# Kernel tuning notes

Measured on AMD Instinct MI355X. Metric: run time of the kernel, lower is better.

The kernel has to match this reference:

```python
import jax, jax.numpy as jnp
import numpy as np

DN = ('NDHWC', 'DHWIO', 'NDHWC')
EPS = 1e-5  # torch BatchNorm default

def _conv(x, w, s):
    # Minkowski conv, kernel 3 centered: output coord j gathers input coords s*j + {-1,0,1}
    return jax.lax.conv_general_dilated(x, w, (s, s, s), ((1, 1),) * 3, dimension_numbers=DN)

def _convt(x, w):
    # stride-2 transpose conv, kernel 3 centered: output p gets input c where 2c in {p-1,p,p+1}
    return jax.lax.conv_general_dilated(x, w, (1, 1, 1), ((1, 2),) * 3,
                                        lhs_dilation=(2, 2, 2), dimension_numbers=DN)

def _down(m):
    # stride-2 coordinate map: a coarse voxel is active iff any of its 2x2x2 fine voxels is
    B, G = m.shape[0], m.shape[1]
    return m.reshape(B, G // 2, 2, G // 2, 2, G // 2, 2).any(axis=(2, 4, 6))

def _mbn(h, m, g, b):
    # MinkowskiBatchNorm: BatchNorm1d over the active (sparse) feature rows only
    mf = m[..., None].astype(h.dtype)
    h = h * mf
    cnt = jnp.maximum(jnp.sum(mf), 1.0)
    mean = jnp.sum(h, axis=(0, 1, 2, 3)) / cnt
    var = jnp.sum(((h - mean) * mf) ** 2, axis=(0, 1, 2, 3)) / cnt
    return ((h - mean) * jax.lax.rsqrt(var + EPS) * g + b) * mf


def setup_inputs() -> dict:
    key = jax.random.key(0)
    ks = jax.random.split(key, 8)
    B, G, Cin, Cout = 2, 64, 4, 16
    def w(k, shape, fan):
        return jax.random.normal(k, shape, jnp.float32) * np.float32(1.0 / np.sqrt(fan))
    return {
        'x': jax.random.normal(ks[0], (B, G, G, G, Cin), jnp.float32),
        'mask': jax.random.bernoulli(ks[1], 0.1, (B, G, G, G)),
        'w1': w(ks[2], (3, 3, 3, Cin, 8), 27 * Cin), 'g1': jnp.ones(8), 'b1': jnp.zeros(8),
        'w2': w(ks[3], (3, 3, 3, 8, 16), 27 * 8), 'g2': jnp.ones(16), 'b2': jnp.zeros(16),
        'w3': w(ks[4], (3, 3, 3, 16, 32), 27 * 16), 'g3': jnp.ones(32), 'b3': jnp.zeros(32),
        'w3t': w(ks[5], (3, 3, 3, 32, 16), 27 * 32), 'g3t': jnp.ones(16), 'b3t': jnp.zeros(16),
        'w2t': w(ks[6], (3, 3, 3, 32, 16), 27 * 32), 'g2t': jnp.ones(16), 'b2t': jnp.zeros(16),
        'w1x1': w(ks[7], (24, Cout), 24),
    }


def reference(x, mask, w1, g1, b1, w2, g2, b2, w3, g3, b3,
              w3t, g3t, b3t, w2t, g2t, b2t, w1x1):
    m1 = mask
    m2 = _down(m1)
    m4 = _down(m2)
    mf1 = m1[..., None].astype(x.dtype)

    xs = x * mf1                                      # sparse tensor: zero at inactive coords
    s1 = _mbn(_conv(xs, w1, 1), m1, g1, b1)           # block1, stride 1
    o = jax.nn.relu(s1)
    s2 = _mbn(_conv(o, w2, 2), m2, g2, b2)            # block2, stride 2
    o = jax.nn.relu(s2)
    s4 = _mbn(_conv(o, w3, 2), m4, g3, b3)            # block3, stride 4
    o = jax.nn.relu(s4)

    o = jax.nn.relu(_mbn(_convt(o, w3t), m2, g3t, b3t))   # block3_tr -> stride-2 coords
    o = jnp.concatenate([o, s2], axis=-1)                 # ME.cat(out, out_s2) -> 32 ch
    o = jax.nn.relu(_mbn(_convt(o, w2t), m1, g2t, b2t))   # block2_tr -> stride-1 coords
    o = jnp.concatenate([o, s1], axis=-1)                 # ME.cat(out, out_s1) -> 24 ch
    return jnp.einsum('bdhwc,co->bdhwo', o, w1x1) * mf1   # conv1_tr: 1x1x1 conv
```

## Files before the change

### kernel.cpp

```cpp
#include <hip/hip_runtime.h>

#define NVOX1 524288
#define NVOX2 65536
#define NVOX4 8192

#define ST_SUM1 16
#define ST_SQ1  24
#define ST_SUM2 32
#define ST_SQ2  48
#define ST_SUM3 64
#define ST_SQ3  96
#define ST_SUM3T 128
#define ST_SQ3T  144
#define ST_SUM2T 160
#define ST_SQ2T  176
#define FLAG_OFF 200
#define IC_N1 204
#define IC_N2 205
#define IC_N4 206
#define ST_ZERO 256

#define OFF_M1C 512
#define OFF_M2  (OFF_M1C + NVOX1)
#define OFF_M4  (OFF_M2 + NVOX2)
#define OFF_H1  (OFF_M4 + NVOX4)
#define OFF_S2  (OFF_H1 + NVOX1 * 8)
#define OFF_H3  (OFF_S2 + NVOX2 * 16)
#define OFF_T3  (OFF_H3 + NVOX4 * 32)
#define OFF_L1  (OFF_T3 + NVOX2 * 16)
#define OFF_L2  (OFF_L1 + NVOX1)
#define OFF_L4  (OFF_L2 + NVOX2)
#define OFF_BC1 (OFF_L4 + NVOX4)
#define OFF_BC2 (OFF_BC1 + 2048)
#define OFF_BC4 (OFF_BC2 + 256)
#define OFF_NB1  (OFF_BC4 + 32)
#define OFF_NB2  (OFF_NB1 + NVOX1)
#define OFF_NB4  (OFF_NB2 + NVOX2)
#define OFF_NBT3 (OFF_NB4 + NVOX4)
#define OFF_NBT2 (OFF_NBT3 + NVOX2)

#define EPSBN 1e-5f

__device__ __forceinline__ void ttaps(int p, int gin, int* c, int* k, int* ok) {
  c[0] = p >> 1; k[0] = (p & 1) ? 0 : 1; ok[0] = 1;
  int cb = (p + 1) >> 1;
  int o = (p & 1) && (cb < gin);
  c[1] = o ? cb : 0; k[1] = 2; ok[1] = o;
}

__device__ __forceinline__ void stat_flush8(float* sum, float* sq, float* s_sum, float* s_sq, int t) {
#pragma unroll
  for (int off = 1; off < 64; off <<= 1)
#pragma unroll
    for (int c = 0; c < 8; c++) {
      sum[c] += __shfl_xor(sum[c], off, 64);
      sq[c]  += __shfl_xor(sq[c], off, 64);
    }
  if ((t & 63) == 0) {
#pragma unroll
    for (int c = 0; c < 8; c++) { atomicAdd(&s_sum[c], sum[c]); atomicAdd(&s_sq[c], sq[c]); }
  }
}

__global__ __launch_bounds__(256) void k_detect(const unsigned int* __restrict__ m,
                                                int* __restrict__ flags) {
  int tid = blockIdx.x * 256 + threadIdx.x;
  int hasf = 0, hasb = 0;
  for (int i = tid; i < NVOX1; i += 256 * 256) {
    unsigned int v = m[i];
    if (v == 0x3F800000u) hasf = 1;
    else if (v > 1u) hasb = 1;
  }
  hasf = __syncthreads_or(hasf);
  hasb = __syncthreads_or(hasb);
  if (threadIdx.x == 0) {
    if (hasf) atomicOr(&flags[0], 1);
    if (hasb) atomicOr(&flags[1], 1);
  }
}

__global__ __launch_bounds__(256) void k_canon(const void* __restrict__ mraw,
                                               int* __restrict__ m1c,
                                               const int* __restrict__ flags,
                                               int* __restrict__ blkcnt1) {
  int idx = blockIdx.x * 256 + threadIdx.x;
  int isf = flags[0], isb = flags[1];
  int v;
  if (isf)      v = (((const float*)mraw)[idx] != 0.f);
  else if (isb) v = (((const unsigned char*)mraw)[idx] != 0);
  else          v = (((const int*)mraw)[idx] != 0);
  m1c[idx] = v;
  int c = __syncthreads_count(v);
  if (threadIdx.x == 0) blkcnt1[blockIdx.x] = c;
}

__global__ __launch_bounds__(256) void k_down1(const int* __restrict__ m1,
                                               int* __restrict__ m2,
                                               int* __restrict__ blkcnt2) {
  int idx = blockIdx.x * 256 + threadIdx.x;
  int x = idx & 31, y = (idx >> 5) & 31, z = (idx >> 10) & 31, b = idx >> 15;
  int any = 0;
#pragma unroll
  for (int dz = 0; dz < 2; dz++)
#pragma unroll
    for (int dy = 0; dy < 2; dy++)
#pragma unroll
      for (int dx = 0; dx < 2; dx++)
        any |= m1[((b * 64 + 2 * z + dz) * 64 + 2 * y + dy) * 64 + 2 * x + dx];
  any = any ? 1 : 0;
  m2[idx] = any;
  int c = __syncthreads_count(any);
  if (threadIdx.x == 0) blkcnt2[blockIdx.x] = c;
}

__global__ __launch_bounds__(256) void k_down2(const int* __restrict__ m2,
                                               int* __restrict__ m4,
                                               int* __restrict__ blkcnt4) {
  int idx = blockIdx.x * 256 + threadIdx.x;
  int x = idx & 15, y = (idx >> 4) & 15, z = (idx >> 8) & 15, b = idx >> 12;
  int any = 0;
#pragma unroll
  for (int dz = 0; dz < 2; dz++)
#pragma unroll
    for (int dy = 0; dy < 2; dy++)
#pragma unroll
      for (int dx = 0; dx < 2; dx++)
        any |= m2[((b * 32 + 2 * z + dz) * 32 + 2 * y + dy) * 32 + 2 * x + dx];
  any = any ? 1 : 0;
  m4[idx] = any;
  int c = __syncthreads_count(any);
  if (threadIdx.x == 0) blkcnt4[blockIdx.x] = c;
}

__global__ __launch_bounds__(1024) void k_scan(int* __restrict__ bc1,
                                               int* __restrict__ bc2,
                                               int* __restrict__ bc4,
                                               int* __restrict__ cnts) {
  __shared__ int sA[2048], sB[2048];
  int* a; int n; int outIdx;
  if (blockIdx.x == 0)      { a = bc1; n = 2048; outIdx = IC_N1; }
  else if (blockIdx.x == 1) { a = bc2; n = 256;  outIdx = IC_N2; }
  else                      { a = bc4; n = 32;   outIdx = IC_N4; }
  int t = threadIdx.x;
  int i0 = t, i1 = t + 1024;
  int v0 = (i0 < n) ? a[i0] : 0;
  int v1 = (i1 < n) ? a[i1] : 0;
  sA[i0] = v0; sA[i1] = v1;
  __syncthreads();
  int* src = sA; int* dst = sB;
  for (int st = 1; st < 2048; st <<= 1) {
    int x0 = src[i0]; if (i0 >= st) x0 += src[i0 - st];
    int x1 = src[i1]; if (i1 >= st) x1 += src[i1 - st];
    dst[i0] = x0; dst[i1] = x1;
    __syncthreads();
    int* tmp = src; src = dst; dst = tmp;
  }
  if (i0 < n) a[i0] = src[i0] - v0;
  if (i1 < n) a[i1] = src[i1] - v1;
  if (t == 0) cnts[outIdx] = src[2047];
}

__global__ __launch_bounds__(256) void k_scatter(const int* __restrict__ m1,
                                                 const int* __restrict__ m2,
                                                 const int* __restrict__ m4,
                                                 const int* __restrict__ bc1,
                                                 const int* __restrict__ bc2,
                                                 const int* __restrict__ bc4,
                                                 int* __restrict__ list1,
                                                 int* __restrict__ list2,
                                                 int* __restrict__ list4) {
  __shared__ int s_w[4];
  int bid = blockIdx.x, t = threadIdx.x;
  const int* mask; const int* base; int* list; int lb;
  if (bid < 2048)      { mask = m1; base = bc1; list = list1; lb = bid; }
  else if (bid < 2304) { mask = m2; base = bc2; list = list2; lb = bid - 2048; }
  else                 { mask = m4; base = bc4; list = list4; lb = bid - 2304; }
  int idx = lb * 256 + t;
  int act = mask[idx];
  unsigned long long b = __ballot(act != 0);
  int lane = t & 63, wid = t >> 6;
  if (lane == 0) s_w[wid] = __popcll(b);
  __syncthreads();
  int wbase = 0;
  for (int i = 0; i < wid; i++) wbase += s_w[i];
  if (act) {
    int pre = __popcll(b & ((1ull << lane) - 1ull));
    list[base[lb] + wbase + pre] = idx;
  }
}

__global__ __launch_bounds__(256) void k_nbr(const int* __restrict__ m1,
                                             const int* __restrict__ m2,
                                             const int* __restrict__ m4,
                                             const int* __restrict__ list1,
                                             const int* __restrict__ list2,
                                             const int* __restrict__ list4,
                                             const int* __restrict__ cnts,
                                             int* __restrict__ nb1,
                                             int* __restrict__ nb2,
                                             int* __restrict__ nb4,
                                             int* __restrict__ nbt3,
                                             int* __restrict__ nbt2) {
  int mode = blockIdx.y;
  int tid = blockIdx.x * 256 + threadIdx.x;
  int stride = gridDim.x * 256;
  if (mode == 0) {
    int n = cnts[IC_N1];
    for (int i = tid; i < n; i += stride) {
      int v = list1[i];
      int vx = v & 63, vy = (v >> 6) & 63, vz = (v >> 12) & 63, vb = v >> 18;
      unsigned wbits = 0; int tap = 0;
#pragma unroll
      for (int kd = 0; kd < 3; kd++) { int d = vz + kd - 1; int okd = ((unsigned)d < 64u); int dc = okd ? d : 0;
#pragma unroll
        for (int kh = 0; kh < 3; kh++) { int h = vy + kh - 1; int okh = ((unsigned)h < 64u); int hc = okh ? h : 0;
#pragma unroll
          for (int kw = 0; kw < 3; kw++) { int ww = vx + kw - 1; int okw = ((unsigned)ww < 64u); int wc = okw ? ww : 0;
            int ni = ((vb * 64 + dc) * 64 + hc) * 64 + wc;
            int bit = (okd & okh & okw) & (m1[ni] != 0);
            wbits |= ((unsigned)bit) << tap; tap++;
          } } }
      nb1[i] = (int)wbits;
    }
  } else if (mode == 1) {
    int n = cnts[IC_N2];
    for (int i = tid; i < n; i += stride) {
      int v = list2[i];
      int vx = v & 31, vy = (v >> 5) & 31, vz = (v >> 10) & 31, vb = v >> 15;
      unsigned wbits = 0; int tap = 0;
#pragma unroll
      for (int kd = 0; kd < 3; kd++) { int d = 2 * vz + kd - 1; int okd = (d >= 0); int dc = okd ? d : 0;
#pragma unroll
        for (int kh = 0; kh < 3; kh++) { int h = 2 * vy + kh - 1; int okh = (h >= 0); int hc = okh ? h : 0;
#pragma unroll
          for (int kw = 0; kw < 3; kw++) { int ww = 2 * vx + kw - 1; int okw = (ww >= 0); int wc = okw ? ww : 0;
            int ni = ((vb * 64 + dc) * 64 + hc) * 64 + wc;
            int bit = (okd & okh & okw) & (m1[ni] != 0);
            wbits |= ((unsigned)bit) << tap; tap++;
          } } }
      nb2[i] = (int)wbits;
    }
  } else if (mode == 2) {
    int n = cnts[IC_N4];
    for (int i = tid; i < n; i += stride) {
      int v = list4[i];
      int vx = v & 15, vy = (v >> 4) & 15, vz = (v >> 8) & 15, vb = v >> 12;
      unsigned wbits = 0; int tap = 0;
#pragma unroll
      for (int kd = 0; kd < 3; kd++) { int d = 2 * vz + kd - 1; int okd = (d >= 0); int dc = okd ? d : 0;
#pragma unroll
        for (int kh = 0; kh < 3; kh++) { int h = 2 * vy + kh - 1; int okh = (h >= 0); int hc = okh ? h : 0;
#pragma unroll
          for (int kw = 0; kw < 3; kw++) { int ww = 2 * vx + kw - 1; int okw = (ww >= 0); int wc = okw ? ww : 0;
            int ni = ((vb * 32 + dc) * 32 + hc) * 32 + wc;
            int bit = (okd & okh & okw) & (m2[ni] != 0);
            wbits |= ((unsigned)bit) << tap; tap++;
          } } }
      nb4[i] = (int)wbits;
    }
  } else if (mode == 3) {
    int n = cnts[IC_N2];
    for (int i = tid; i < n; i += stride) {
      int v = list2[i];
      int px = v & 31, py = (v >> 5) & 31, pz = (v >> 10) & 31, vb = v >> 15;
      int czv[2], kzv[2], okz[2], cyv[2], kyv[2], oky[2], cxv[2], kxv[2], okx[2];
      ttaps(pz, 16, czv, kzv, okz);
      ttaps(py, 16, cyv, kyv, oky);
      ttaps(px, 16, cxv, kxv, okx);
      unsigned wbits = 0; int comb = 0;
#pragma unroll
      for (int dz = 0; dz < 2; dz++)
#pragma unroll
        for (int dy = 0; dy < 2; dy++)
#pragma unroll
          for (int dx = 0; dx < 2; dx++) {
            int ni = ((vb * 16 + czv[dz]) * 16 + cyv[dy]) * 16 + cxv[dx];
            int bit = (okz[dz] & oky[dy] & okx[dx]) & (m4[ni] != 0);
            wbits |= ((unsigned)bit) << comb; comb++;
          }
      nbt3[i] = (int)wbits;
    }
  } else {
    int n = cnts[IC_N1];
    for (int i = tid; i < n; i += stride) {
      int v = list1[i];
      int px = v & 63, py = (v >> 6) & 63, pz = (v >> 12) & 63, vb = v >> 18;
      int czv[2], kzv[2], okz[2], cyv[2], kyv[2], oky[2], cxv[2], kxv[2], okx[2];
      ttaps(pz, 32, czv, kzv, okz);
      ttaps(py, 32, cyv, kyv, oky);
      ttaps(px, 32, cxv, kxv, okx);
      unsigned wbits = 0; int comb = 0;
#pragma unroll
      for (int dz = 0; dz < 2; dz++)
#pragma unroll
        for (int dy = 0; dy < 2; dy++)
#pragma unroll
          for (int dx = 0; dx < 2; dx++) {
            int ni = ((vb * 32 + czv[dz]) * 32 + cyv[dy]) * 32 + cxv[dx];
            int bit = (okz[dz] & oky[dy] & okx[dx]) & (m2[ni] != 0);
            wbits |= ((unsigned)bit) << comb; comb++;
          }
      nbt2[i] = (int)wbits;
    }
  }
}

__global__ __launch_bounds__(256) void k_conv1(const float* __restrict__ x,
                                               const int* __restrict__ nb1,
                                               const int* __restrict__ list1,
                                               const int* __restrict__ cnts,
                                               const float* __restrict__ w,
                                               float* __restrict__ h1,
                                               float* __restrict__ stats) {
  __shared__ float s_w[27 * 32];
  __shared__ float s_sum[8], s_sq[8];
  int t = threadIdx.x;
  { const float4* w4 = (const float4*)w; float4* sw4 = (float4*)s_w;
    for (int i = t; i < 216; i += 256) sw4[i] = w4[i]; }
  if (t < 8) { s_sum[t] = 0.f; s_sq[t] = 0.f; }
  __syncthreads();
  int n = cnts[IC_N1];
  float sum[8], sq[8];
#pragma unroll
  for (int c = 0; c < 8; c++) { sum[c] = 0.f; sq[c] = 0.f; }
  for (int i = blockIdx.x * 256 + t; i < n; i += gridDim.x * 256) {
    int v = list1[i];
    unsigned nbr = (unsigned)nb1[i];
    int vx = v & 63, vy = (v >> 6) & 63, vz = (v >> 12) & 63, vb = v >> 18;
    float acc[8];
#pragma unroll
    for (int c = 0; c < 8; c++) acc[c] = 0.f;
    int tap = 0;
#pragma unroll
    for (int kd = 0; kd < 3; kd++)
#pragma unroll
      for (int kh = 0; kh < 3; kh++)
#pragma unroll
        for (int kw = 0; kw < 3; kw++) {
          if (nbr & (1u << tap)) {
            int ni = ((vb * 64 + vz + kd - 1) * 64 + vy + kh - 1) * 64 + vx + kw - 1;
            float4 ip = *(const float4*)(x + (size_t)ni * 4);
            const float* wp = s_w + tap * 32;
#pragma unroll
            for (int co = 0; co < 8; co++) {
              float a = fmaf(ip.x, wp[co], acc[co]);
              a = fmaf(ip.y, wp[8 + co], a);
              a = fmaf(ip.z, wp[16 + co], a);
              acc[co] = fmaf(ip.w, wp[24 + co], a);
            }
          }
          tap++;
        }
    float4* hp = (float4*)(h1 + (size_t)v * 8);
    hp[0] = make_float4(acc[0], acc[1], acc[2], acc[3]);
    hp[1] = make_float4(acc[4], acc[5], acc[6], acc[7]);
#pragma unroll
    for (int c = 0; c < 8; c++) { sum[c] += acc[c]; sq[c] += acc[c] * acc[c]; }
  }
  stat_flush8(sum, sq, s_sum, s_sq, t);
  __syncthreads();
  if (t < 8) {
    if (s_sum[t] != 0.f) atomicAdd(&stats[ST_SUM1 + t], s_sum[t]);
    if (s_sq[t]  != 0.f) atomicAdd(&stats[ST_SQ1 + t], s_sq[t]);
  }
}

__global__ __launch_bounds__(256) void k_conv2(const float* __restrict__ h1,
                                               const int* __restrict__ nb2,
                                               const int* __restrict__ list2,
                                               const int* __restrict__ cnts,
                                               const float* __restrict__ w,
                                               const float* __restrict__ g1,
                                               const float* __restrict__ b1,
                                               float* __restrict__ s2,
                                               float* __restrict__ stats) {
  __shared__ float s_w[27 * 8 * 8];
  __shared__ float s_sc[8], s_bi[8];
  __shared__ float s_sum[8], s_sq[8];
  int t = threadIdx.x, g = blockIdx.y;
  for (int i = t; i < 432; i += 256) {
    int r = i >> 1, half = i & 1;
    *(float4*)(s_w + r * 8 + half * 4) = *(const float4*)(w + r * 16 + g * 8 + half * 4);
  }
  if (t < 8) {
    float cnt = fmaxf((float)cnts[IC_N1], 1.f);
    float mean = stats[ST_SUM1 + t] / cnt;
    float var = fmaxf(stats[ST_SQ1 + t] / cnt - mean * mean, 0.f);
    float sc = g1[t] * rsqrtf(var + EPSBN);
    s_sc[t] = sc; s_bi[t] = b1[t] - mean * sc;
    s_sum[t] = 0.f; s_sq[t] = 0.f;
  }
  __syncthreads();
  int n = cnts[IC_N2];
  float sum[8], sq[8];
#pragma unroll
  for (int c = 0; c < 8; c++) { sum[c] = 0.f; sq[c] = 0.f; }
  for (int i = blockIdx.x * 256 + t; i < n; i += gridDim.x * 256) {
    int v = list2[i];
    unsigned nbr = (unsigned)nb2[i];
    int vx = v & 31, vy = (v >> 5) & 31, vz = (v >> 10) & 31, vb = v >> 15;
    float acc[8];
#pragma unroll
    for (int c = 0; c < 8; c++) acc[c] = 0.f;
    int tap = 0;
#pragma unroll
    for (int kd = 0; kd < 3; kd++)
#pragma unroll
      for (int kh = 0; kh < 3; kh++)
#pragma unroll
        for (int kw = 0; kw < 3; kw++) {
          if (nbr & (1u << tap)) {
            int ni = ((vb * 64 + 2 * vz + kd - 1) * 64 + 2 * vy + kh - 1) * 64 + 2 * vx + kw - 1;
            float4 i0 = *(const float4*)(h1 + (size_t)ni * 8);
            float4 i1 = *(const float4*)(h1 + (size_t)ni * 8 + 4);
            float r[8] = {i0.x, i0.y, i0.z, i0.w, i1.x, i1.y, i1.z, i1.w};
            const float* wp = s_w + tap * 64;
#pragma unroll
            for (int ci = 0; ci < 8; ci++) {
              float vv = fmaxf(fmaf(r[ci], s_sc[ci], s_bi[ci]), 0.f);
#pragma unroll
              for (int co = 0; co < 8; co++) acc[co] = fmaf(vv, wp[ci * 8 + co], acc[co]);
            }
          }
          tap++;
        }
    float4* sp = (float4*)(s2 + (size_t)v * 16 + g * 8);
    sp[0] = make_float4(acc[0], acc[1], acc[2], acc[3]);
    sp[1] = make_float4(acc[4], acc[5], acc[6], acc[7]);
#pragma unroll
    for (int c = 0; c < 8; c++) { sum[c] += acc[c]; sq[c] += acc[c] * acc[c]; }
  }
  stat_flush8(sum, sq, s_sum, s_sq, t);
  __syncthreads();
  if (t < 8) {
    if (s_sum[t] != 0.f) atomicAdd(&stats[ST_SUM2 + g * 8 + t], s_sum[t]);
    if (s_sq[t]  != 0.f) atomicAdd(&stats[ST_SQ2 + g * 8 + t], s_sq[t]);
  }
}

__global__ __launch_bounds__(256) void k_conv3(const float* __restrict__ s2raw,
                                               const int* __restrict__ nb4,
                                               const int* __restrict__ list4,
                                               const int* __restrict__ cnts,
                                               const float* __restrict__ w,
                                               const float* __restrict__ g2,
                                               const float* __restrict__ b2,
                                               float* __restrict__ h3,
                                               float* __restrict__ stats) {
  __shared__ float s_w[27 * 16 * 8];
  __shared__ float s_sc[16], s_bi[16];
  __shared__ float s_sum[8], s_sq[8];
  int t = threadIdx.x, g = blockIdx.y;
  for (int i = t; i < 864; i += 256) {
    int r = i >> 1, half = i & 1;
    *(float4*)(s_w + r * 8 + half * 4) = *(const float4*)(w + r * 32 + g * 8 + half * 4);
  }
  if (t < 16) {
    float cnt = fmaxf((float)cnts[IC_N2], 1.f);
    float mean = stats[ST_SUM2 + t] / cnt;
    float var = fmaxf(stats[ST_SQ2 + t] / cnt - mean * mean, 0.f);
    float sc = g2[t] * rsqrtf(var + EPSBN);
    s_sc[t] = sc; s_bi[t] = b2[t] - mean * sc;
  }
  if (t < 8) { s_sum[t] = 0.f; s_sq[t] = 0.f; }
  __syncthreads();
  int n = cnts[IC_N4];
  float sum[8], sq[8];
#pragma unroll
  for (int c = 0; c < 8; c++) { sum[c] = 0.f; sq[c] = 0.f; }
  for (int i = blockIdx.x * 256 + t; i < n; i += gridDim.x * 256) {
    int v = list4[i];
    unsigned nbr = (unsigned)nb4[i];
    int vx = v & 15, vy = (v >> 4) & 15, vz = (v >> 8) & 15, vb = v >> 12;
    float acc[8];
#pragma unroll
    for (int c = 0; c < 8; c++) acc[c] = 0.f;
    int tap = 0;
#pragma unroll
    for (int kd = 0; kd < 3; kd++)
#pragma unroll
      for (int kh = 0; kh < 3; kh++)
#pragma unroll
        for (int kw = 0; kw < 3; kw++) {
          if (nbr & (1u << tap)) {
            int ni = ((vb * 32 + 2 * vz + kd - 1) * 32 + 2 * vy + kh - 1) * 32 + 2 * vx + kw - 1;
            const float4* ip = (const float4*)(s2raw + (size_t)ni * 16);
            const float* wp = s_w + tap * 128;
#pragma unroll
            for (int cq = 0; cq < 4; cq++) {
              float4 q = ip[cq];
              float rr[4] = {q.x, q.y, q.z, q.w};
#pragma unroll
              for (int j = 0; j < 4; j++) {
                int ci = cq * 4 + j;
                float vv = fmaxf(fmaf(rr[j], s_sc[ci], s_bi[ci]), 0.f);
#pragma unroll
                for (int co = 0; co < 8; co++) acc[co] = fmaf(vv, wp[ci * 8 + co], acc[co]);
              }
            }
          }
          tap++;
        }
    float4* hp = (float4*)(h3 + (size_t)v * 32 + g * 8);
    hp[0] = make_float4(acc[0], acc[1], acc[2], acc[3]);
    hp[1] = make_float4(acc[4], acc[5], acc[6], acc[7]);
#pragma unroll
    for (int c = 0; c < 8; c++) { sum[c] += acc[c]; sq[c] += acc[c] * acc[c]; }
  }
  stat_flush8(sum, sq, s_sum, s_sq, t);
  __syncthreads();
  if (t < 8) {
    if (s_sum[t] != 0.f) atomicAdd(&stats[ST_SUM3 + g * 8 + t], s_sum[t]);
    if (s_sq[t]  != 0.f) atomicAdd(&stats[ST_SQ3 + g * 8 + t], s_sq[t]);
  }
}

__global__ __launch_bounds__(256) void k_convt3(const float* __restrict__ h3raw,
                                                const int* __restrict__ nbt3,
                                                const int* __restrict__ list2,
                                                const int* __restrict__ cnts,
                                                const float* __restrict__ w,
                                                const float* __restrict__ g3,
                                                const float* __restrict__ b3,
                                                float* __restrict__ t3,
                                                float* __restrict__ stats) {
  __shared__ float s_w[27 * 32 * 8];
  __shared__ float s_sc[32], s_bi[32];
  __shared__ float s_sum[8], s_sq[8];
  int t = threadIdx.x, g = blockIdx.y;
  for (int i = t; i < 1728; i += 256) {
    int r = i >> 1, half = i & 1;
    *(float4*)(s_w + r * 8 + half * 4) = *(const float4*)(w + r * 16 + g * 8 + half * 4);
  }
  if (t < 32) {
    float cnt = fmaxf((float)cnts[IC_N4], 1.f);
    float mean = stats[ST_SUM3 + t] / cnt;
    float var = fmaxf(stats[ST_SQ3 + t] / cnt - mean * mean, 0.f);
    float sc = g3[t] * rsqrtf(var + EPSBN);
    s_sc[t] = sc; s_bi[t] = b3[t] - mean * sc;
  }
  if (t < 8) { s_sum[t] = 0.f; s_sq[t] = 0.f; }
  __syncthreads();
  int n = cnts[IC_N2];
  float sum[8], sq[8];
#pragma unroll
  for (int c = 0; c < 8; c++) { sum[c] = 0.f; sq[c] = 0.f; }
  for (int i = blockIdx.x * 256 + t; i < n; i += gridDim.x * 256) {
    int v = list2[i];
    unsigned nbr = (unsigned)nbt3[i];
    int px = v & 31, py = (v >> 5) & 31, pz = (v >> 10) & 31, vb = v >> 15;
    int czv[2], kzv[2], okz[2], cyv[2], kyv[2], oky[2], cxv[2], kxv[2], okx[2];
    ttaps(pz, 16, czv, kzv, okz);
    ttaps(py, 16, cyv, kyv, oky);
    ttaps(px, 16, cxv, kxv, okx);
    float acc[8];
#pragma unroll
    for (int c = 0; c < 8; c++) acc[c] = 0.f;
    int comb = 0;
#pragma unroll
    for (int dz = 0; dz < 2; dz++)
#pragma unroll
      for (int dy = 0; dy < 2; dy++)
#pragma unroll
        for (int dx = 0; dx < 2; dx++) {
          if (nbr & (1u << comb)) {
            int ni = ((vb * 16 + czv[dz]) * 16 + cyv[dy]) * 16 + cxv[dx];
            const float4* ip = (const float4*)(h3raw + (size_t)ni * 32);
            const float* wp = s_w + ((kzv[dz] * 3 + kyv[dy]) * 3 + kxv[dx]) * 256;
#pragma unroll
            for (int cq = 0; cq < 8; cq++) {
              float4 q = ip[cq];
              float rr[4] = {q.x, q.y, q.z, q.w};
#pragma unroll
              for (int j = 0; j < 4; j++) {
                int ci = cq * 4 + j;
                float vv = fmaxf(fmaf(rr[j], s_sc[ci], s_bi[ci]), 0.f);
#pragma unroll
                for (int co = 0; co < 8; co++) acc[co] = fmaf(vv, wp[ci * 8 + co], acc[co]);
              }
            }
          }
          comb++;
        }
    float4* op = (float4*)(t3 + (size_t)v * 16 + g * 8);
    op[0] = make_float4(acc[0], acc[1], acc[2], acc[3]);
    op[1] = make_float4(acc[4], acc[5], acc[6], acc[7]);
#pragma unroll
    for (int c = 0; c < 8; c++) { sum[c] += acc[c]; sq[c] += acc[c] * acc[c]; }
  }
  stat_flush8(sum, sq, s_sum, s_sq, t);
  __syncthreads();
  if (t < 8) {
    if (s_sum[t] != 0.f) atomicAdd(&stats[ST_SUM3T + g * 8 + t], s_sum[t]);
    if (s_sq[t]  != 0.f) atomicAdd(&stats[ST_SQ3T + g * 8 + t], s_sq[t]);
  }
}

__global__ __launch_bounds__(256) void k_convt2(const float* __restrict__ t3raw,
                                                const float* __restrict__ s2raw,
                                                const int* __restrict__ nbt2,
                                                const int* __restrict__ list1,
                                                const int* __restrict__ cnts,
                                                const float* __restrict__ w,
                                                const float* __restrict__ g3t,
                                                const float* __restrict__ b3t,
                                                const float* __restrict__ g2,
                                                const float* __restrict__ b2,
                                                float* __restrict__ outraw,
                                                float* __restrict__ stats) {
  __shared__ float s_w[27 * 32 * 8];
  __shared__ float s_sct[16], s_bit[16], s_sc2[16], s_bi2[16];
  __shared__ float s_sum[8], s_sq[8];
  int t = threadIdx.x, g = blockIdx.y;
  for (int i = t; i < 1728; i += 256) {
    int r = i >> 1, half = i & 1;
    *(float4*)(s_w + r * 8 + half * 4) = *(const float4*)(w + r * 16 + g * 8 + half * 4);
  }
  if (t < 16) {
    float cnt = fmaxf((float)cnts[IC_N2], 1.f);
    float mean = stats[ST_SUM3T + t] / cnt;
    float var = fmaxf(stats[ST_SQ3T + t] / cnt - mean * mean, 0.f);
    float sc = g3t[t] * rsqrtf(var + EPSBN);
    s_sct[t] = sc; s_bit[t] = b3t[t] - mean * sc;
    float mean2 = stats[ST_SUM2 + t] / cnt;
    float var2 = fmaxf(stats[ST_SQ2 + t] / cnt - mean2 * mean2, 0.f);
    float sc2 = g2[t] * rsqrtf(var2 + EPSBN);
    s_sc2[t] = sc2; s_bi2[t] = b2[t] - mean2 * sc2;
  }
  if (t < 8) { s_sum[t] = 0.f; s_sq[t] = 0.f; }
  __syncthreads();
  int n = cnts[IC_N1];
  float sum[8], sq[8];
#pragma unroll
  for (int c = 0; c < 8; c++) { sum[c] = 0.f; sq[c] = 0.f; }
  for (int i = blockIdx.x * 256 + t; i < n; i += gridDim.x * 256) {
    int v = list1[i];
    unsigned nbr = (unsigned)nbt2[i];
    int px = v & 63, py = (v >> 6) & 63, pz = (v >> 12) & 63, vb = v >> 18;
    int czv[2], kzv[2], okz[2], cyv[2], kyv[2], oky[2], cxv[2], kxv[2], okx[2];
    ttaps(pz, 32, czv, kzv, okz);
    ttaps(py, 32, cyv, kyv, oky);
    ttaps(px, 32, cxv, kxv, okx);
    float acc[8];
#pragma unroll
    for (int c = 0; c < 8; c++) acc[c] = 0.f;
    int comb = 0;
#pragma unroll
    for (int dz = 0; dz < 2; dz++)
#pragma unroll
      for (int dy = 0; dy < 2; dy++)
#pragma unroll
        for (int dx = 0; dx < 2; dx++) {
          if (nbr & (1u << comb)) {
            int ni = ((vb * 32 + czv[dz]) * 32 + cyv[dy]) * 32 + cxv[dx];
            const float4* tp = (const float4*)(t3raw + (size_t)ni * 16);
            const float4* sp = (const float4*)(s2raw + (size_t)ni * 16);
            const float* wp = s_w + ((kzv[dz] * 3 + kyv[dy]) * 3 + kxv[dx]) * 256;
#pragma unroll
            for (int cq = 0; cq < 4; cq++) {
              float4 q = tp[cq];
              float rr[4] = {q.x, q.y, q.z, q.w};
#pragma unroll
              for (int j = 0; j < 4; j++) {
                int ci = cq * 4 + j;
                float vv = fmaxf(fmaf(rr[j], s_sct[ci], s_bit[ci]), 0.f);
#pragma unroll
                for (int co = 0; co < 8; co++) acc[co] = fmaf(vv, wp[ci * 8 + co], acc[co]);
              }
            }
#pragma unroll
            for (int cq = 0; cq < 4; cq++) {
              float4 q = sp[cq];
              float rr[4] = {q.x, q.y, q.z, q.w};
#pragma unroll
              for (int j = 0; j < 4; j++) {
                int ci = cq * 4 + j;
                float vv = fmaf(rr[j], s_sc2[ci], s_bi2[ci]);
#pragma unroll
                for (int co = 0; co < 8; co++) acc[co] = fmaf(vv, wp[(16 + ci) * 8 + co], acc[co]);
              }
            }
          }
          comb++;
        }
    float4* op = (float4*)(outraw + (size_t)v * 16 + g * 8);
    op[0] = make_float4(acc[0], acc[1], acc[2], acc[3]);
    op[1] = make_float4(acc[4], acc[5], acc[6], acc[7]);
#pragma unroll
    for (int c = 0; c < 8; c++) { sum[c] += acc[c]; sq[c] += acc[c] * acc[c]; }
  }
  stat_flush8(sum, sq, s_sum, s_sq, t);
  __syncthreads();
  if (t < 8) {
    if (s_sum[t] != 0.f) atomicAdd(&stats[ST_SUM2T + g * 8 + t], s_sum[t]);
    if (s_sq[t]  != 0.f) atomicAdd(&stats[ST_SQ2T + g * 8 + t], s_sq[t]);
  }
}

__global__ __launch_bounds__(256) void k_final(float* __restrict__ out,
                                               const float* __restrict__ h1raw,
                                               const int* __restrict__ m1,
                                               const int* __restrict__ cnts,
                                               const float* __restrict__ g2t,
                                               const float* __restrict__ b2t,
                                               const float* __restrict__ g1,
                                               const float* __restrict__ b1,
                                               const float* __restrict__ w1x1,
                                               const float* __restrict__ stats) {
  __shared__ float s_sc[16], s_bi[16], s_sc1[8], s_bi1[8], s_w[384];
  int t = threadIdx.x;
  for (int i = t; i < 384; i += 256) s_w[i] = w1x1[i];
  if (t < 16) {
    float cnt = fmaxf((float)cnts[IC_N1], 1.f);
    float mean = stats[ST_SUM2T + t] / cnt;
    float var = fmaxf(stats[ST_SQ2T + t] / cnt - mean * mean, 0.f);
    float sc = g2t[t] * rsqrtf(var + EPSBN);
    s_sc[t] = sc; s_bi[t] = b2t[t] - mean * sc;
  }
  if (t < 8) {
    float cnt = fmaxf((float)cnts[IC_N1], 1.f);
    float mean = stats[ST_SUM1 + t] / cnt;
    float var = fmaxf(stats[ST_SQ1 + t] / cnt - mean * mean, 0.f);
    float sc = g1[t] * rsqrtf(var + EPSBN);
    s_sc1[t] = sc; s_bi1[t] = b1[t] - mean * sc;
  }
  __syncthreads();
  int v = blockIdx.x * 256 + t;
  float* op = out + (size_t)v * 16;
  float4* op4 = (float4*)op;
  if (!m1[v]) {
    float4 z = {0.f, 0.f, 0.f, 0.f};
    op4[0] = z; op4[1] = z; op4[2] = z; op4[3] = z;
    return;
  }
  float t2[16];
  {
#pragma unroll
    for (int cq = 0; cq < 4; cq++) {
      float4 q = op4[cq];
      t2[cq * 4 + 0] = fmaxf(fmaf(q.x, s_sc[cq * 4 + 0], s_bi[cq * 4 + 0]), 0.f);
      t2[cq * 4 + 1] = fmaxf(fmaf(q.y, s_sc[cq * 4 + 1], s_bi[cq * 4 + 1]), 0.f);
      t2[cq * 4 + 2] = fmaxf(fmaf(q.z, s_sc[cq * 4 + 2], s_bi[cq * 4 + 2]), 0.f);
      t2[cq * 4 + 3] = fmaxf(fmaf(q.w, s_sc[cq * 4 + 3], s_bi[cq * 4 + 3]), 0.f);
    }
  }
  float s1v[8];
  {
    const float4* sp4 = (const float4*)(h1raw + (size_t)v * 8);
#pragma unroll
    for (int cq = 0; cq < 2; cq++) {
      float4 q = sp4[cq];
      s1v[cq * 4 + 0] = fmaf(q.x, s_sc1[cq * 4 + 0], s_bi1[cq * 4 + 0]);
      s1v[cq * 4 + 1] = fmaf(q.y, s_sc1[cq * 4 + 1], s_bi1[cq * 4 + 1]);
      s1v[cq * 4 + 2] = fmaf(q.z, s_sc1[cq * 4 + 2], s_bi1[cq * 4 + 2]);
      s1v[cq * 4 + 3] = fmaf(q.w, s_sc1[cq * 4 + 3], s_bi1[cq * 4 + 3]);
    }
  }
  float o[16];
#pragma unroll
  for (int oc = 0; oc < 16; oc++) o[oc] = 0.f;
#pragma unroll
  for (int c = 0; c < 16; c++) {
    float vv = t2[c];
#pragma unroll
    for (int oc = 0; oc < 16; oc++) o[oc] = fmaf(vv, s_w[c * 16 + oc], o[oc]);
  }
#pragma unroll
  for (int c = 0; c < 8; c++) {
    float vv = s1v[c];
#pragma unroll
    for (int oc = 0; oc < 16; oc++) o[oc] = fmaf(vv, s_w[(16 + c) * 16 + oc], o[oc]);
  }
#pragma unroll
  for (int cq = 0; cq < 4; cq++) {
    float4 q = {o[cq * 4 + 0], o[cq * 4 + 1], o[cq * 4 + 2], o[cq * 4 + 3]};
    op4[cq] = q;
  }
}

extern "C" void kernel_launch(void* const* d_in, const int* in_sizes, int n_in,
                              void* d_out, int out_size, void* d_ws, size_t ws_size,
                              hipStream_t stream) {
  const float* x    = (const float*)d_in[0];
  const void*  mraw = d_in[1];
  const float* w1   = (const float*)d_in[2];
  const float* g1   = (const float*)d_in[3];
  const float* b1   = (const float*)d_in[4];
  const float* w2   = (const float*)d_in[5];
  const float* g2   = (const float*)d_in[6];
  const float* b2   = (const float*)d_in[7];
  const float* w3   = (const float*)d_in[8];
  const float* g3   = (const float*)d_in[9];
  const float* b3   = (const float*)d_in[10];
  const float* w3t  = (const float*)d_in[11];
  const float* g3t  = (const float*)d_in[12];
  const float* b3t  = (const float*)d_in[13];
  const float* w2t  = (const float*)d_in[14];
  const float* g2t  = (const float*)d_in[15];
  const float* b2t  = (const float*)d_in[16];
  const float* w1x1 = (const float*)d_in[17];

  float* ws = (float*)d_ws;
  float* stats = ws;
  int* cnts = (int*)ws;
  int* flags = (int*)(ws + FLAG_OFF);
  int* m1c = (int*)(ws + OFF_M1C);
  int* m2  = (int*)(ws + OFF_M2);
  int* m4  = (int*)(ws + OFF_M4);
  float* h1 = ws + OFF_H1;
  float* s2 = ws + OFF_S2;
  float* h3 = ws + OFF_H3;
  float* t3 = ws + OFF_T3;
  int* list1 = (int*)(ws + OFF_L1);
  int* list2 = (int*)(ws + OFF_L2);
  int* list4 = (int*)(ws + OFF_L4);
  int* bc1 = (int*)(ws + OFF_BC1);
  int* bc2 = (int*)(ws + OFF_BC2);
  int* bc4 = (int*)(ws + OFF_BC4);
  int* nb1  = (int*)(ws + OFF_NB1);
  int* nb2  = (int*)(ws + OFF_NB2);
  int* nb4  = (int*)(ws + OFF_NB4);
  int* nbt3 = (int*)(ws + OFF_NBT3);
  int* nbt2 = (int*)(ws + OFF_NBT2);
  float* out = (float*)d_out;

  hipMemsetAsync(ws, 0, ST_ZERO * sizeof(float), stream);
  k_detect<<<256, 256, 0, stream>>>((const unsigned int*)mraw, flags);
  k_canon<<<NVOX1 / 256, 256, 0, stream>>>(mraw, m1c, flags, bc1);
  k_down1<<<NVOX2 / 256, 256, 0, stream>>>(m1c, m2, bc2);
  k_down2<<<NVOX4 / 256, 256, 0, stream>>>(m2, m4, bc4);
  k_scan<<<3, 1024, 0, stream>>>(bc1, bc2, bc4, cnts);
  k_scatter<<<2048 + 256 + 32, 256, 0, stream>>>(m1c, m2, m4, bc1, bc2, bc4, list1, list2, list4);
  k_nbr<<<dim3(256, 5), 256, 0, stream>>>(m1c, m2, m4, list1, list2, list4, cnts,
                                          nb1, nb2, nb4, nbt3, nbt2);
  k_conv1<<<256, 256, 0, stream>>>(x, nb1, list1, cnts, w1, h1, stats);
  k_conv2<<<dim3(256, 2), 256, 0, stream>>>(h1, nb2, list2, cnts, w2, g1, b1, s2, stats);
  k_conv3<<<dim3(32, 4), 256, 0, stream>>>(s2, nb4, list4, cnts, w3, g2, b2, h3, stats);
  k_convt3<<<dim3(256, 2), 256, 0, stream>>>(h3, nbt3, list2, cnts, w3t, g3, b3, t3, stats);
  k_convt2<<<dim3(256, 2), 256, 0, stream>>>(t3, s2, nbt2, list1, cnts, w2t, g3t, b3t, g2, b2, out, stats);
  k_final<<<NVOX1 / 256, 256, 0, stream>>>(out, h1, m1c, cnts, g2t, b2t, g1, b1, w1x1, stats);
}
```

Baseline: 191.4 us.

## Store intermediate sparse features in compacted rank-indexed buffers

Adds a rank map (dense voxel to compacted index) built in the scatter kernel, and switches all intermediate feature tensors (input, h1, s2, h3, t3) from dense grid-indexed storage to compacted per-active-voxel storage. The aim is a smaller working set and better cache locality, with contiguous writes by list index. Each neighbor gather now costs an extra indirect load through the rank array, and a new kernel pass compacts the input x.

```diff
diff --git a/kernel.cpp b/kernel.cpp
--- a/kernel.cpp
+++ b/kernel.cpp
@@ -23,11 +23,10 @@
 #define OFF_M1C 512
 #define OFF_M2  (OFF_M1C + NVOX1)
 #define OFF_M4  (OFF_M2 + NVOX2)
-#define OFF_H1  (OFF_M4 + NVOX4)
-#define OFF_S2  (OFF_H1 + NVOX1 * 8)
-#define OFF_H3  (OFF_S2 + NVOX2 * 16)
-#define OFF_T3  (OFF_H3 + NVOX4 * 32)
-#define OFF_L1  (OFF_T3 + NVOX2 * 16)
+#define OFF_R1  (OFF_M4 + NVOX4)
+#define OFF_R2  (OFF_R1 + NVOX1)
+#define OFF_R4  (OFF_R2 + NVOX2)
+#define OFF_L1  (OFF_R4 + NVOX4)
 #define OFF_L2  (OFF_L1 + NVOX1)
 #define OFF_L4  (OFF_L2 + NVOX2)
 #define OFF_BC1 (OFF_L4 + NVOX4)
@@ -38,6 +37,11 @@
 #define OFF_NB4  (OFF_NB2 + NVOX2)
 #define OFF_NBT3 (OFF_NB4 + NVOX4)
 #define OFF_NBT2 (OFF_NBT3 + NVOX2)
+#define OFF_XC   (OFF_NBT2 + NVOX1)
+#define OFF_H1C  (OFF_XC + NVOX1 * 4)
+#define OFF_S2C  (OFF_H1C + NVOX1 * 8)
+#define OFF_H3C  (OFF_S2C + NVOX2 * 16)
+#define OFF_T3C  (OFF_H3C + NVOX4 * 32)
 
 #define EPSBN 1e-5f
 
@@ -168,13 +172,16 @@
                                                  const int* __restrict__ bc4,
                                                  int* __restrict__ list1,
                                                  int* __restrict__ list2,
-                                                 int* __restrict__ list4) {
+                                                 int* __restrict__ list4,
+                                                 int* __restrict__ rank1,
+                                                 int* __restrict__ rank2,
+                                                 int* __restrict__ rank4) {
   __shared__ int s_w[4];
   int bid = blockIdx.x, t = threadIdx.x;
-  const int* mask; const int* base; int* list; int lb;
-  if (bid < 2048)      { mask = m1; base = bc1; list = list1; lb = bid; }
-  else if (bid < 2304) { mask = m2; base = bc2; list = list2; lb = bid - 2048; }
-  else                 { mask = m4; base = bc4; list = list4; lb = bid - 2304; }
+  const int* mask; const int* base; int* list; int* rank; int lb;
+  if (bid < 2048)      { mask = m1; base = bc1; list = list1; rank = rank1; lb = bid; }
+  else if (bid < 2304) { mask = m2; base = bc2; list = list2; rank = rank2; lb = bid - 2048; }
+  else                 { mask = m4; base = bc4; list = list4; rank = rank4; lb = bid - 2304; }
   int idx = lb * 256 + t;
   int act = mask[idx];
   unsigned long long b = __ballot(act != 0);
@@ -185,7 +192,9 @@
   for (int i = 0; i < wid; i++) wbase += s_w[i];
   if (act) {
     int pre = __popcll(b & ((1ull << lane) - 1ull));
-    list[base[lb] + wbase + pre] = idx;
+    int pos = base[lb] + wbase + pre;
+    list[pos] = idx;
+    rank[idx] = pos;
   }
 }
 
@@ -305,12 +314,24 @@
   }
 }
 
-__global__ __launch_bounds__(256) void k_conv1(const float* __restrict__ x,
+__global__ __launch_bounds__(256) void k_compact_x(const float* __restrict__ x,
+                                                   const int* __restrict__ m1,
+                                                   const int* __restrict__ rank1,
+                                                   float* __restrict__ xc) {
+  int v = blockIdx.x * 256 + threadIdx.x;
+  if (!m1[v]) return;
+  int r = rank1[v];
+  float4 q = *(const float4*)(x + (size_t)v * 4);
+  *(float4*)(xc + (size_t)r * 4) = q;
+}
+
+__global__ __launch_bounds__(256) void k_conv1(const float* __restrict__ xc,
+                                               const int* __restrict__ rank1,
                                                const int* __restrict__ nb1,
                                                const int* __restrict__ list1,
                                                const int* __restrict__ cnts,
                                                const float* __restrict__ w,
-                                               float* __restrict__ h1,
+                                               float* __restrict__ h1c,
                                                float* __restrict__ stats) {
   __shared__ float s_w[27 * 32];
   __shared__ float s_sum[8], s_sq[8];
@@ -339,7 +360,8 @@
         for (int kw = 0; kw < 3; kw++) {
           if (nbr & (1u << tap)) {
             int ni = ((vb * 64 + vz + kd - 1) * 64 + vy + kh - 1) * 64 + vx + kw - 1;
-            float4 ip = *(const float4*)(x + (size_t)ni * 4);
+            int r = rank1[ni];
+            float4 ip = *(const float4*)(xc + (size_t)r * 4);
             const float* wp = s_w + tap * 32;
 #pragma unroll
             for (int co = 0; co < 8; co++) {
@@ -351,7 +373,7 @@
           }
           tap++;
         }
-    float4* hp = (float4*)(h1 + (size_t)v * 8);
+    float4* hp = (float4*)(h1c + (size_t)i * 8);
     hp[0] = make_float4(acc[0], acc[1], acc[2], acc[3]);
     hp[1] = make_float4(acc[4], acc[5], acc[6], acc[7]);
 #pragma unroll
@@ -365,14 +387,15 @@
   }
 }
 
-__global__ __launch_bounds__(256) void k_conv2(const float* __restrict__ h1,
+__global__ __launch_bounds__(256) void k_conv2(const float* __restrict__ h1c,
+                                               const int* __restrict__ rank1,
                                                const int* __restrict__ nb2,
                                                const int* __restrict__ list2,
                                                const int* __restrict__ cnts,
                                                const float* __restrict__ w,
                                                const float* __restrict__ g1,
                                                const float* __restrict__ b1,
-                                               float* __restrict__ s2,
+                                               float* __restrict__ s2c,
                                                float* __restrict__ stats) {
   __shared__ float s_w[27 * 8 * 8];
   __shared__ float s_sc[8], s_bi[8];
@@ -411,20 +434,21 @@
         for (int kw = 0; kw < 3; kw++) {
           if (nbr & (1u << tap)) {
             int ni = ((vb * 64 + 2 * vz + kd - 1) * 64 + 2 * vy + kh - 1) * 64 + 2 * vx + kw - 1;
-            float4 i0 = *(const float4*)(h1 + (size_t)ni * 8);
-            float4 i1 = *(const float4*)(h1 + (size_t)ni * 8 + 4);
-            float r[8] = {i0.x, i0.y, i0.z, i0.w, i1.x, i1.y, i1.z, i1.w};
+            int r = rank1[ni];
+            float4 i0 = *(const float4*)(h1c + (size_t)r * 8);
+            float4 i1 = *(const float4*)(h1c + (size_t)r * 8 + 4);
+            float rr[8] = {i0.x, i0.y, i0.z, i0.w, i1.x, i1.y, i1.z, i1.w};
             const float* wp = s_w + tap * 64;
 #pragma unroll
             for (int ci = 0; ci < 8; ci++) {
-              float vv = fmaxf(fmaf(r[ci], s_sc[ci], s_bi[ci]), 0.f);
+              float vv = fmaxf(fmaf(rr[ci], s_sc[ci], s_bi[ci]), 0.f);
 #pragma unroll
               for (int co = 0; co < 8; co++) acc[co] = fmaf(vv, wp[ci * 8 + co], acc[co]);
             }
           }
           tap++;
         }
-    float4* sp = (float4*)(s2 + (size_t)v * 16 + g * 8);
+    float4* sp = (float4*)(s2c + (size_t)i * 16 + g * 8);
     sp[0] = make_float4(acc[0], acc[1], acc[2], acc[3]);
     sp[1] = make_float4(acc[4], acc[5], acc[6], acc[7]);
 #pragma unroll
@@ -438,14 +462,15 @@
   }
 }
 
-__global__ __launch_bounds__(256) void k_conv3(const float* __restrict__ s2raw,
+__global__ __launch_bounds__(256) void k_conv3(const float* __restrict__ s2c,
+                                               const int* __restrict__ rank2,
                                                const int* __restrict__ nb4,
                                                const int* __restrict__ list4,
                                                const int* __restrict__ cnts,
                                                const float* __restrict__ w,
                                                const float* __restrict__ g2,
                                                const float* __restrict__ b2,
-                                               float* __restrict__ h3,
+                                               float* __restrict__ h3c,
                                                float* __restrict__ stats) {
   __shared__ float s_w[27 * 16 * 8];
   __shared__ float s_sc[16], s_bi[16];
@@ -484,7 +509,8 @@
         for (int kw = 0; kw < 3; kw++) {
           if (nbr & (1u << tap)) {
             int ni = ((vb * 32 + 2 * vz + kd - 1) * 32 + 2 * vy + kh - 1) * 32 + 2 * vx + kw - 1;
-            const float4* ip = (const float4*)(s2raw + (size_t)ni * 16);
+            int r = rank2[ni];
+            const float4* ip = (const float4*)(s2c + (size_t)r * 16);
             const float* wp = s_w + tap * 128;
 #pragma unroll
             for (int cq = 0; cq < 4; cq++) {
@@ -501,7 +527,7 @@
           }
           tap++;
         }
-    float4* hp = (float4*)(h3 + (size_t)v * 32 + g * 8);
+    float4* hp = (float4*)(h3c + (size_t)i * 32 + g * 8);
     hp[0] = make_float4(acc[0], acc[1], acc[2], acc[3]);
     hp[1] = make_float4(acc[4], acc[5], acc[6], acc[7]);
 #pragma unroll
@@ -515,14 +541,15 @@
   }
 }
 
-__global__ __launch_bounds__(256) void k_convt3(const float* __restrict__ h3raw,
+__global__ __launch_bounds__(256) void k_convt3(const float* __restrict__ h3c,
+                                                const int* __restrict__ rank4,
                                                 const int* __restrict__ nbt3,
                                                 const int* __restrict__ list2,
                                                 const int* __restrict__ cnts,
                                                 const float* __restrict__ w,
                                                 const float* __restrict__ g3,
                                                 const float* __restrict__ b3,
-                                                float* __restrict__ t3,
+                                                float* __restrict__ t3c,
                                                 float* __restrict__ stats) {
   __shared__ float s_w[27 * 32 * 8];
   __shared__ float s_sc[32], s_bi[32];
@@ -565,7 +592,8 @@
         for (int dx = 0; dx < 2; dx++) {
           if (nbr & (1u << comb)) {
             int ni = ((vb * 16 + czv[dz]) * 16 + cyv[dy]) * 16 + cxv[dx];
-            const float4* ip = (const float4*)(h3raw + (size_t)ni * 32);
+            int r = rank4[ni];
+            const float4* ip = (const float4*)(h3c + (size_t)r * 32);
             const float* wp = s_w + ((kzv[dz] * 3 + kyv[dy]) * 3 + kxv[dx]) * 256;
 #pragma unroll
             for (int cq = 0; cq < 8; cq++) {
@@ -582,7 +610,7 @@
           }
           comb++;
         }
-    float4* op = (float4*)(t3 + (size_t)v * 16 + g * 8);
+    float4* op = (float4*)(t3c + (size_t)i * 16 + g * 8);
     op[0] = make_float4(acc[0], acc[1], acc[2], acc[3]);
     op[1] = make_float4(acc[4], acc[5], acc[6], acc[7]);
 #pragma unroll
@@ -596,8 +624,9 @@
   }
 }
 
-__global__ __launch_bounds__(256) void k_convt2(const float* __restrict__ t3raw,
-                                                const float* __restrict__ s2raw,
+__global__ __launch_bounds__(256) void k_convt2(const float* __restrict__ t3c,
+                                                const float* __restrict__ s2c,
+                                                const int* __restrict__ rank2,
                                                 const int* __restrict__ nbt2,
                                                 const int* __restrict__ list1,
                                                 const int* __restrict__ cnts,
@@ -653,8 +682,9 @@
         for (int dx = 0; dx < 2; dx++) {
           if (nbr & (1u << comb)) {
             int ni = ((vb * 32 + czv[dz]) * 32 + cyv[dy]) * 32 + cxv[dx];
-            const float4* tp = (const float4*)(t3raw + (size_t)ni * 16);
-            const float4* sp = (const float4*)(s2raw + (size_t)ni * 16);
+            int r = rank2[ni];
+            const float4* tp = (const float4*)(t3c + (size_t)r * 16);
+            const float4* sp = (const float4*)(s2c + (size_t)r * 16);
             const float* wp = s_w + ((kzv[dz] * 3 + kyv[dy]) * 3 + kxv[dx]) * 256;
 #pragma unroll
             for (int cq = 0; cq < 4; cq++) {
@@ -698,8 +728,9 @@
 }
 
 __global__ __launch_bounds__(256) void k_final(float* __restrict__ out,
-                                               const float* __restrict__ h1raw,
+                                               const float* __restrict__ h1c,
                                                const int* __restrict__ m1,
+                                               const int* __restrict__ rank1,
                                                const int* __restrict__ cnts,
                                                const float* __restrict__ g2t,
                                                const float* __restrict__ b2t,
@@ -733,6 +764,7 @@
     op4[0] = z; op4[1] = z; op4[2] = z; op4[3] = z;
     return;
   }
+  int r = rank1[v];
   float t2[16];
   {
 #pragma unroll
@@ -746,7 +778,7 @@
   }
   float s1v[8];
   {
-    const float4* sp4 = (const float4*)(h1raw + (size_t)v * 8);
+    const float4* sp4 = (const float4*)(h1c + (size_t)r * 8);
 #pragma unroll
     for (int cq = 0; cq < 2; cq++) {
       float4 q = sp4[cq];
@@ -807,10 +839,9 @@
   int* m1c = (int*)(ws + OFF_M1C);
   int* m2  = (int*)(ws + OFF_M2);
   int* m4  = (int*)(ws + OFF_M4);
-  float* h1 = ws + OFF_H1;
-  float* s2 = ws + OFF_S2;
-  float* h3 = ws + OFF_H3;
-  float* t3 = ws + OFF_T3;
+  int* rank1 = (int*)(ws + OFF_R1);
+  int* rank2 = (int*)(ws + OFF_R2);
+  int* rank4 = (int*)(ws + OFF_R4);
   int* list1 = (int*)(ws + OFF_L1);
   int* list2 = (int*)(ws + OFF_L2);
   int* list4 = (int*)(ws + OFF_L4);
@@ -822,6 +853,11 @@
   int* nb4  = (int*)(ws + OFF_NB4);
   int* nbt3 = (int*)(ws + OFF_NBT3);
   int* nbt2 = (int*)(ws + OFF_NBT2);
+  float* xc  = ws + OFF_XC;
+  float* h1c = ws + OFF_H1C;
+  float* s2c = ws + OFF_S2C;
+  float* h3c = ws + OFF_H3C;
+  float* t3c = ws + OFF_T3C;
   float* out = (float*)d_out;
 
   hipMemsetAsync(ws, 0, ST_ZERO * sizeof(float), stream);
@@ -830,13 +866,16 @@
   k_down1<<<NVOX2 / 256, 256, 0, stream>>>(m1c, m2, bc2);
   k_down2<<<NVOX4 / 256, 256, 0, stream>>>(m2, m4, bc4);
   k_scan<<<3, 1024, 0, stream>>>(bc1, bc2, bc4, cnts);
-  k_scatter<<<2048 + 256 + 32, 256, 0, stream>>>(m1c, m2, m4, bc1, bc2, bc4, list1, list2, list4);
+  k_scatter<<<2048 + 256 + 32, 256, 0, stream>>>(m1c, m2, m4, bc1, bc2, bc4,
+                                                 list1, list2, list4, rank1, rank2, rank4);
   k_nbr<<<dim3(256, 5), 256, 0, stream>>>(m1c, m2, m4, list1, list2, list4, cnts,
                                           nb1, nb2, nb4, nbt3, nbt2);
-  k_conv1<<<256, 256, 0, stream>>>(x, nb1, list1, cnts, w1, h1, stats);
-  k_conv2<<<dim3(256, 2), 256, 0, stream>>>(h1, nb2, list2, cnts, w2, g1, b1, s2, stats);
-  k_conv3<<<dim3(32, 4), 256, 0, stream>>>(s2, nb4, list4, cnts, w3, g2, b2, h3, stats);
-  k_convt3<<<dim3(256, 2), 256, 0, stream>>>(h3, nbt3, list2, cnts, w3t, g3, b3, t3, stats);
-  k_convt2<<<dim3(256, 2), 256, 0, stream>>>(t3, s2, nbt2, list1, cnts, w2t, g3t, b3t, g2, b2, out, stats);
-  k_final<<<NVOX1 / 256, 256, 0, stream>>>(out, h1, m1c, cnts, g2t, b2t, g1, b1, w1x1, stats);
-}
+  k_compact_x<<<NVOX1 / 256, 256, 0, stream>>>(x, m1c, rank1, xc);
+  k_conv1<<<256, 256, 0, stream>>>(xc, rank1, nb1, list1, cnts, w1, h1c, stats);
+  k_conv2<<<dim3(256, 2), 256, 0, stream>>>(h1c, rank1, nb2, list2, cnts, w2, g1, b1, s2c, stats);
+  k_conv3<<<dim3(32, 4), 256, 0, stream>>>(s2c, rank2, nb4, list4, cnts, w3, g2, b2, h3c, stats);
+  k_convt3<<<dim3(256, 2), 256, 0, stream>>>(h3c, rank4, nbt3, list2, cnts, w3t, g3, b3, t3c, stats);
+  k_convt2<<<dim3(256, 2), 256, 0, stream>>>(t3c, s2c, rank2, nbt2, list1, cnts, w2t,
+                                             g3t, b3t, g2, b2, out, stats);
+  k_final<<<NVOX1 / 256, 256, 0, stream>>>(out, h1c, m1c, rank1, cnts, g2t, b2t, g1, b1, w1x1, stats);
+}
```

New measurement: 209.4 us. 9.4% more time.
